# Optimization experiments

Measured on AMD Instinct MI355X. Metric: run time of the kernel, lower is better.

## Reference

```python
import jax, jax.numpy as jnp
import numpy as np

B, N, K = 16, 2048, 16        # events, nodes per event, neighbors
F_IN, L = 64, 64              # in_size, layer_size
EPS = 1e-5                    # BatchNorm1d eps


def setup_inputs() -> dict:
    key = jax.random.key(0)
    k1, k2 = jax.random.split(key, 2)
    x = jax.random.normal(k1, (B * N, F_IN), jnp.float32)
    batch = jnp.repeat(jnp.arange(B, dtype=jnp.int32), N)  # equal-size events
    W = jax.random.normal(k2, (2 * F_IN, L), jnp.float32) * 0.08
    b = jnp.zeros((L,), jnp.float32)
    gamma = jnp.ones((L,), jnp.float32)
    beta = jnp.zeros((L,), jnp.float32)
    return {"x": x, "batch": batch, "W": W, "b": b, "gamma": gamma, "beta": beta}


def reference(x, batch, W, b, gamma, beta):
    # batch encodes B equal-size events -> reshape to [B, N, F]
    xr = x.reshape(B, N, F_IN)

    # dynamic kNN in feature space, per event (self included, as in PyG knn)
    sq = jnp.sum(xr * xr, axis=-1)                                  # [B, N]
    d = sq[:, :, None] + sq[:, None, :] - 2.0 * jnp.einsum(
        'bnf,bmf->bnm', xr, xr)                                     # [B, N, N]
    _, idx = jax.lax.top_k(-d, K)                                   # [B, N, K]

    # gather neighbor features
    xj = jax.vmap(lambda xe, ie: xe[ie])(xr, idx)                   # [B, N, K, F]
    xi = jnp.broadcast_to(xr[:, :, None, :], (B, N, K, F_IN))

    # EdgeConv message: nn(cat([x_i, x_j - x_i]))
    e = jnp.concatenate([xi, xj - xi], axis=-1)                     # [B, N, K, 2F]
    h = jnp.einsum('bnke,el->bnkl', e, W) + b                       # Linear

    # BatchNorm1d over all edges (training-mode batch stats, biased var)
    m = jnp.mean(h, axis=(0, 1, 2))
    v = jnp.var(h, axis=(0, 1, 2))
    h = (h - m) * jax.lax.rsqrt(v + EPS) * gamma + beta
    h = jax.nn.relu(h)

    # aggr='mean' over the K neighbors
    out = jnp.mean(h, axis=2)                                       # [B, N, L]
    return out.reshape(B * N, L)
```

## Files before the change

### kernel.cpp

```cpp
#include <hip/hip_runtime.h>
#include <hip/hip_fp16.h>
#include <math.h>

#define B_EV    16
#define N_NODES 2048
#define K_NN    16
#define F_IN    64
#define L_OUT   64
#define NT      (B_EV * N_NODES)
#define EDGES   (NT * K_NN)

typedef __attribute__((ext_vector_type(8)))  short bh8;
typedef __attribute__((ext_vector_type(16))) float f32x16;
typedef __attribute__((ext_vector_type(8)))  unsigned short us8;

__device__ inline unsigned short bf16_rne(float f) {
  unsigned int u = __float_as_uint(f);
  return (unsigned short)((u + 0x7FFFu + ((u >> 16) & 1u)) >> 16);
}
__device__ inline float bf16f(unsigned short h) {
  return __uint_as_float(((unsigned int)h) << 16);
}

__device__ inline void gload16(const void* g, void* l) {
  __builtin_amdgcn_global_load_lds(
      (const __attribute__((address_space(1))) void*)(g),
      (__attribute__((address_space(3))) void*)(l), 16, 0, 0);
}

__global__ __launch_bounds__(256) void k_uv(const float* __restrict__ x,
                                            const float* __restrict__ W,
                                            float* __restrict__ u,
                                            float* __restrict__ v,
                                            float* __restrict__ sq,
                                            unsigned short* __restrict__ xh,
                                            unsigned short* __restrict__ xl) {
  __shared__ float xs[64][64];
  const int t = threadIdx.x;
  const int l = t & 63, g = t >> 6;
  const int nodeBase = blockIdx.x * 64;

  {
    const float4* gx = (const float4*)(x + (size_t)nodeBase * 64);
    float4* lx = (float4*)&xs[0][0];
    #pragma unroll
    for (int p = 0; p < 4; ++p) lx[p * 256 + t] = gx[p * 256 + t];
  }
  float wdc[64], w2c[64];
  #pragma unroll
  for (int f = 0; f < 64; ++f) {
    float w1v = W[f * 64 + l];
    float w2v = W[4096 + f * 64 + l];
    wdc[f] = w1v - w2v;
    w2c[f] = w2v;
  }
  __syncthreads();

  #pragma unroll
  for (int p = 0; p < 2; ++p) {
    int n = p * 32 + (t >> 3), j = t & 7;
    float xv = xs[n][j];
    float s = __fmul_rn(xv, xv);
    #pragma unroll
    for (int i = 1; i < 8; ++i) {
      float c = xs[n][j + 8 * i];
      s = __fadd_rn(s, __fmul_rn(c, c));
    }
    s = __fadd_rn(s, __shfl_xor(s, 1));
    s = __fadd_rn(s, __shfl_xor(s, 2));
    s = __fadd_rn(s, __shfl_xor(s, 4));
    if (j == 0) sq[nodeBase + n] = s;
  }
  #pragma unroll
  for (int p = 0; p < 4; ++p) {
    int i = p * 256 + t;
    float4 vv = ((const float4*)&xs[0][0])[i];
    ushort4 h, lo;
    h.x = bf16_rne(vv.x); lo.x = bf16_rne(vv.x - bf16f(h.x));
    h.y = bf16_rne(vv.y); lo.y = bf16_rne(vv.y - bf16f(h.y));
    h.z = bf16_rne(vv.z); lo.z = bf16_rne(vv.z - bf16f(h.z));
    h.w = bf16_rne(vv.w); lo.w = bf16_rne(vv.w - bf16f(h.w));
    ((ushort4*)xh)[(size_t)nodeBase * 16 + i] = h;
    ((ushort4*)xl)[(size_t)nodeBase * 16 + i] = lo;
  }

  for (int rep = 0; rep < 16; ++rep) {
    int n = rep * 4 + g;
    const float4* xr = (const float4*)xs[n];
    float au = 0.f, av = 0.f;
    #pragma unroll
    for (int fq = 0; fq < 16; ++fq) {
      float4 xv = xr[fq];
      au = fmaf(xv.x, wdc[fq * 4 + 0], au); av = fmaf(xv.x, w2c[fq * 4 + 0], av);
      au = fmaf(xv.y, wdc[fq * 4 + 1], au); av = fmaf(xv.y, w2c[fq * 4 + 1], av);
      au = fmaf(xv.z, wdc[fq * 4 + 2], au); av = fmaf(xv.z, w2c[fq * 4 + 2], av);
      au = fmaf(xv.w, wdc[fq * 4 + 3], au); av = fmaf(xv.w, w2c[fq * 4 + 3], av);
    }
    u[(size_t)(nodeBase + n) * 64 + l] = au;
    v[(size_t)(nodeBase + n) * 64 + l] = av;
  }
}

__global__ __launch_bounds__(256, 6) void k_gemm(const unsigned short* __restrict__ xh,
                                                 const unsigned short* __restrict__ xl,
                                                 const float* __restrict__ sq,
                                                 unsigned short* __restrict__ Sbuf,
                                                 int evBase) {
  __shared__ char xb[16384];
  __shared__ __align__(16) unsigned short Sh[32 * 128];
  const int t    = threadIdx.x;
  const int w    = t >> 6;
  const int lane = t & 63;
  const int ev    = evBase + (blockIdx.x >> 7);
  const int rem   = blockIdx.x & 127;
  const int strip = rem >> 1;
  const int half  = rem & 1;
  const int rowBase = strip * 32;
  const int T0 = half * 8;
  const size_t evNode = (size_t)ev * N_NODES;
  const float* __restrict__ sqev = sq + evNode;
  unsigned short* __restrict__ Sev =
      Sbuf + (size_t)(ev - evBase) * N_NODES * N_NODES;
  char* Sc = (char*)Sh;

  {
    int col = t >> 3;
    int fbs = ((t & 7) << 4) ^ ((col & 7) << 4);
    gload16((const char*)(xh + (evNode + rowBase + col) * 64) + fbs, Sc + t * 16);
    gload16((const char*)(xl + (evNode + rowBase + col) * 64) + fbs, Sc + 4096 + t * 16);
    #pragma unroll
    for (int p = 0; p < 4; ++p) {
      const int colB = p * 32 + (t >> 3);
      const char* g = (const char*)(xh + (evNode + T0 * 128 + colB) * 64) + fbs;
      gload16(g, xb + p * 4096 + t * 16);
    }
  }
  __syncthreads();
  bh8 ah[4], al[4];
  {
    int row = lane & 31;
    int fb  = (lane >> 5) * 16;
    #pragma unroll
    for (int ks = 0; ks < 4; ++ks) {
      int off = (row * 128 + ks * 32 + fb) ^ ((row & 7) << 4);
      ah[ks] = *(const bh8*)(Sc + off);
      al[ks] = *(const bh8*)(Sc + 4096 + off);
    }
  }
  __syncthreads();

  for (int T = T0; T < T0 + 8; ++T) {
    const int tileCol = T * 128;
    {
      f32x16 acc;
      #pragma unroll
      for (int q = 0; q < 16; ++q) acc[q] = 0.f;
      int colIn = w * 32 + (lane & 31);
      int fb = (lane >> 5) * 16;
      #pragma unroll
      for (int ks = 0; ks < 4; ++ks) {
        int off = (colIn * 128 + ks * 32 + fb) ^ ((colIn & 7) << 4);
        bh8 bh = *(const bh8*)(xb + off);
        acc = __builtin_amdgcn_mfma_f32_32x32x16_bf16(ah[ks], bh, acc, 0, 0, 0);
        acc = __builtin_amdgcn_mfma_f32_32x32x16_bf16(al[ks], bh, acc, 0, 0, 0);
      }
      float sqc = sqev[tileCol + colIn];
      #pragma unroll
      for (int reg = 0; reg < 16; ++reg) {
        int m = (reg & 3) + 8 * (reg >> 2) + 4 * (lane >> 5);
        Sh[m * 128 + colIn] =
            __half_as_ushort(__float2half(fmaf(-2.0f, acc[reg], sqc)));
      }
    }
    __syncthreads();
    if (T < T0 + 7) {
      #pragma unroll
      for (int p = 0; p < 4; ++p) {
        const int colB = p * 32 + (t >> 3);
        const int fbs = ((t & 7) << 4) ^ (((t >> 3) & 7) << 4);
        const char* g = (const char*)(xh + (evNode + tileCol + 128 + colB) * 64) + fbs;
        gload16(g, xb + p * 4096 + t * 16);
      }
    }
    {
      int r  = t >> 3;
      int cg = t & 7;
      unsigned short* gS =
          Sev + (size_t)(rowBase + r) * N_NODES + tileCol + cg * 16;
      const uint4* lS = (const uint4*)(Sh + r * 128 + cg * 16);
      *(uint4*)gS = lS[0];
      *(uint4*)(gS + 8) = lS[1];
    }
    __syncthreads();
  }
}

#define SCR_CAP 192
#define SEL_DELTA 1.0f

__global__ __launch_bounds__(256, 1) void k_sel(const float* __restrict__ x,
                                                const float* __restrict__ sq,
                                                const unsigned short* __restrict__ Sbuf,
                                                int* __restrict__ nidx,
                                                int rowBase) {
  __shared__ float xiS[4][64];
  __shared__ int candLDS[4][SCR_CAP];
  __shared__ unsigned long long keysLDS[4][SCR_CAP];
  const int w = threadIdx.x >> 6, lane = threadIdx.x & 63;
  const int rowInChunk = blockIdx.x * 4 + w;
  const int grow = rowBase + rowInChunk;
  const int ev = grow >> 11;
  const int rowInEv = grow & 2047;
  const size_t evNode = (size_t)ev * N_NODES;
  const unsigned short* __restrict__ Srow = Sbuf + (size_t)rowInChunk * N_NODES;
  const float* __restrict__ sqev = sq + evNode;
  const float* __restrict__ xev = x + evNode * F_IN;

  xiS[w][lane] = x[(evNode + rowInEv) * F_IN + lane];

  us8 pk[4];
  #pragma unroll
  for (int q = 0; q < 4; ++q)
    pk[q] = *(const us8*)(Srow + q * 512 + lane * 8);

  float mn = 3.4e38f;
  #pragma unroll
  for (int q = 0; q < 4; ++q) {
    #pragma unroll
    for (int e = 0; e < 8; ++e)
      mn = fminf(mn, __half2float(__ushort_as_half(pk[q][e])));
  }
  #pragma unroll
  for (int k = 2; k <= 64; k <<= 1) {
    #pragma unroll
    for (int j = k >> 1; j >= 1; j >>= 1) {
      float o = __shfl_xor(mn, j);
      bool up = ((lane & k) == 0);
      bool iAmLower = ((lane & j) == 0);
      bool wantSmall = (up == iAmLower);
      bool less = (mn < o);
      if (less != wantSmall) mn = o;
    }
  }
  const float thr = __shfl(mn, 15) + SEL_DELTA;

  unsigned int msk[4];
  int c = 0;
  #pragma unroll
  for (int q = 0; q < 4; ++q) {
    unsigned int m = 0;
    #pragma unroll
    for (int e = 0; e < 8; ++e) {
      float v = __half2float(__ushort_as_half(pk[q][e]));
      m |= (v <= thr) ? (1u << e) : 0u;
    }
    msk[q] = m;
    c += __popc(m);
  }
  int incl = c;
  #pragma unroll
  for (int off = 1; off < 64; off <<= 1) {
    int n = __shfl_up(incl, off);
    if (lane >= off) incl += n;
  }
  int pos = incl - c;
  int total = __shfl(incl, 63);
  const int cn = (total < SCR_CAP) ? total : SCR_CAP;
  #pragma unroll
  for (int q = 0; q < 4; ++q) {
    unsigned int m = msk[q];
    while (m) {
      int e = __ffs(m) - 1;
      m &= m - 1;
      if (pos < SCR_CAP) candLDS[w][pos] = q * 512 + lane * 8 + e;
      ++pos;
    }
  }

  const float sqn = sqev[rowInEv];
  const float* xiW = xiS[w];
  const int* crow = candLDS[w];

  int base = 0;
  while (base < cn) {
    int rem = cn - base;
    if (rem <= 32) {
      int hf = lane >> 5;
      int ii = lane & 31;
      int ci = base + ii;
      bool act = ii < rem;
      int mcol = act ? crow[ci] : 0;
      const float4* xm = (const float4*)(xev + (size_t)mcol * F_IN);
      double d0 = 0.0, d1 = 0.0;
      #pragma unroll
      for (int q = 0; q < 8; ++q) {
        int fq = hf * 8 + q;
        float4 cc = xm[fq];
        float4 xq = *(const float4*)(xiW + fq * 4);
        d0 = fma((double)xq.x, (double)cc.x, d0);
        d1 = fma((double)xq.y, (double)cc.y, d1);
        d0 = fma((double)xq.z, (double)cc.z, d0);
        d1 = fma((double)xq.w, (double)cc.w, d1);
      }
      double ds = d0 + d1;
      double od = __shfl_xor(ds, 32);
      if (act && hf == 0) {
        float dot32 = (float)(ds + od);
        float sv = __fsub_rn(__fadd_rn(sqn, sqev[mcol]), __fmul_rn(2.0f, dot32));
        unsigned int fb = __float_as_uint(sv);
        fb = (fb & 0x80000000u) ? ~fb : (fb | 0x80000000u);
        keysLDS[w][ci] = ((unsigned long long)fb << 32) | (unsigned int)mcol;
      }
      base = cn;
    } else {
      int ci = base + lane;
      bool act = ci < cn;
      int mcol = act ? crow[ci] : 0;
      const float4* xm = (const float4*)(xev + (size_t)mcol * F_IN);
      double d0 = 0.0, d1 = 0.0, d2 = 0.0, d3 = 0.0;
      #pragma unroll
      for (int fq = 0; fq < 16; fq += 4) {
        float4 c0 = xm[fq + 0], c1 = xm[fq + 1], c2 = xm[fq + 2], c3 = xm[fq + 3];
        float4 x0 = *(const float4*)(xiW + fq * 4);
        float4 x1 = *(const float4*)(xiW + fq * 4 + 4);
        float4 x2 = *(const float4*)(xiW + fq * 4 + 8);
        float4 x3 = *(const float4*)(xiW + fq * 4 + 12);
        d0 = fma((double)x0.x, (double)c0.x, d0);
        d0 = fma((double)x0.y, (double)c0.y, d0);
        d0 = fma((double)x0.z, (double)c0.z, d0);
        d0 = fma((double)x0.w, (double)c0.w, d0);
        d1 = fma((double)x1.x, (double)c1.x, d1);
        d1 = fma((double)x1.y, (double)c1.y, d1);
        d1 = fma((double)x1.z, (double)c1.z, d1);
        d1 = fma((double)x1.w, (double)c1.w, d1);
        d2 = fma((double)x2.x, (double)c2.x, d2);
        d2 = fma((double)x2.y, (double)c2.y, d2);
        d2 = fma((double)x2.z, (double)c2.z, d2);
        d2 = fma((double)x2.w, (double)c2.w, d2);
        d3 = fma((double)x3.x, (double)c3.x, d3);
        d3 = fma((double)x3.y, (double)c3.y, d3);
        d3 = fma((double)x3.z, (double)c3.z, d3);
        d3 = fma((double)x3.w, (double)c3.w, d3);
      }
      if (act) {
        float dot32 = (float)((d0 + d1) + (d2 + d3));
        float sv = __fsub_rn(__fadd_rn(sqn, sqev[mcol]), __fmul_rn(2.0f, dot32));
        unsigned int fb = __float_as_uint(sv);
        fb = (fb & 0x80000000u) ? ~fb : (fb | 0x80000000u);
        keysLDS[w][ci] = ((unsigned long long)fb << 32) | (unsigned int)mcol;
      }
      base += 64;
    }
  }

  const unsigned long long INVALID = ~0ull;
  unsigned long long k0 = INVALID, k1 = INVALID, k2 = INVALID;
  if (lane < cn)        k0 = keysLDS[w][lane];
  if (lane + 64 < cn)   k1 = keysLDS[w][lane + 64];
  if (lane + 128 < cn)  k2 = keysLDS[w][lane + 128];
  int r0 = 0, r1 = 0, r2 = 0;
  for (int i = 0; i < cn; ++i) {
    unsigned long long kk = keysLDS[w][i];
    r0 += (kk < k0) ? 1 : 0;
    r1 += (kk < k1) ? 1 : 0;
    r2 += (kk < k2) ? 1 : 0;
  }
  const size_t outBase = (evNode + rowInEv) * K_NN;
  if (lane < cn && r0 < K_NN)
    nidx[outBase + r0] = (int)evNode + (int)(k0 & 0x7FFFFFFFu);
  if (lane + 64 < cn && r1 < K_NN)
    nidx[outBase + r1] = (int)evNode + (int)(k1 & 0x7FFFFFFFu);
  if (lane + 128 < cn && r2 < K_NN)
    nidx[outBase + r2] = (int)evNode + (int)(k2 & 0x7FFFFFFFu);
}

#define NS 16
#define NC 128
union KnnSmem {
  struct {
    char  xb[32768];
    float S[32 * 129];
  } a;
  struct {
    float sc[32][NC + 1];
    int   id[32][NC + 1];
    int   cand[32][24];
    float resc[32][24];
  } b;
};

__global__ __launch_bounds__(256, 3) void k_knn(const float* __restrict__ x,
                                                const unsigned short* __restrict__ xh,
                                                const unsigned short* __restrict__ xl,
                                                const float* __restrict__ sq,
                                                int* __restrict__ nidx) {
  __shared__ KnnSmem sm;
  const int t    = threadIdx.x;
  const int r    = t & 31;
  const int c8   = t >> 5;
  const int w    = t >> 6;
  const int lane = t & 63;
  const int ev    = blockIdx.x >> 6;
  const int strip = blockIdx.x & 63;
  const int rowBase = strip * 32;
  const size_t evNode = (size_t)ev * N_NODES;
  const float* __restrict__ sqev = sq + evNode;

  {
    int col = t >> 3;
    int fb  = (t & 7) << 4;
    const char* gh = (const char*)(xh + (evNode + rowBase + col) * 64) + fb;
    const char* gl = (const char*)(xl + (evNode + rowBase + col) * 64) + fb;
    int off = (col * 128 + fb) ^ ((col & 7) << 4);
    *(uint4*)(sm.a.xb + off)         = *(const uint4*)gh;
    *(uint4*)(sm.a.xb + 16384 + off) = *(const uint4*)gl;
  }
  __syncthreads();
  bh8 ah[4], al[4];
  {
    int row = lane & 31;
    int fb  = (lane >> 5) * 16;
    #pragma unroll
    for (int ks = 0; ks < 4; ++ks) {
      int off = (row * 128 + ks * 32 + fb) ^ ((row & 7) << 4);
      ah[ks] = *(const bh8*)(sm.a.xb + off);
      al[ks] = *(const bh8*)(sm.a.xb + 16384 + off);
    }
  }

  float dist[NS]; int idxk[NS];
  #pragma unroll
  for (int q = 0; q < NS; ++q) { dist[q] = 3.4e38f; idxk[q] = 0x7FFFFFFF; }
  float curMax = 3.4e38f;

  for (int T = 0; T < 16; ++T) {
    __syncthreads();
    const int tileCol = T * 128;
    #pragma unroll
    for (int p = 0; p < 8; ++p) {
      int idx16 = (p & 3) * 256 + t;
      int col = idx16 >> 3;
      int fb  = (idx16 & 7) << 4;
      const unsigned short* src = (p < 4) ? xh : xl;
      const char* g = (const char*)(src + (evNode + tileCol + col) * 64) + fb;
      int off = ((p < 4) ? 0 : 16384) + ((col * 128 + fb) ^ ((col & 7) << 4));
      *(uint4*)(sm.a.xb + off) = *(const uint4*)g;
    }
    __syncthreads();
    {
      f32x16 acc;
      #pragma unroll
      for (int q = 0; q < 16; ++q) acc[q] = 0.f;
      int colIn = w * 32 + (lane & 31);
      int fb = (lane >> 5) * 16;
      #pragma unroll
      for (int ks = 0; ks < 4; ++ks) {
        int off = (colIn * 128 + ks * 32 + fb) ^ ((colIn & 7) << 4);
        bh8 bh = *(const bh8*)(sm.a.xb + off);
        bh8 bl = *(const bh8*)(sm.a.xb + 16384 + off);
        acc = __builtin_amdgcn_mfma_f32_32x32x16_bf16(ah[ks], bh, acc, 0, 0, 0);
        acc = __builtin_amdgcn_mfma_f32_32x32x16_bf16(ah[ks], bl, acc, 0, 0, 0);
        acc = __builtin_amdgcn_mfma_f32_32x32x16_bf16(al[ks], bh, acc, 0, 0, 0);
      }
      float sqc = sqev[tileCol + colIn];
      #pragma unroll
      for (int reg = 0; reg < 16; ++reg) {
        int m = (reg & 3) + 8 * (reg >> 2) + 4 * (lane >> 5);
        sm.a.S[m * 129 + colIn] = fmaf(-2.0f, acc[reg], sqc);
      }
    }
    __syncthreads();
    for (int j = 0; j < 16; ++j) {
      int cIn = c8 * 16 + j;
      float s = sm.a.S[r * 129 + cIn];
      if (s <= curMax) {
        int col = tileCol + cIn;
        float bv = dist[0]; int bi = idxk[0]; int slot = 0;
        #pragma unroll
        for (int q = 1; q < NS; ++q) {
          bool worse = (dist[q] > bv) || ((dist[q] == bv) && (idxk[q] > bi));
          slot = worse ? q : slot;
          bv = worse ? dist[q] : bv;
          bi = worse ? idxk[q] : bi;
        }
        if ((s < bv) || ((s == bv) && (col < bi))) {
          #pragma unroll
          for (int q = 0; q < NS; ++q) {
            dist[q] = (q == slot) ? s : dist[q];
            idxk[q] = (q == slot) ? col : idxk[q];
          }
          float cm = dist[0];
          #pragma unroll
          for (int q = 1; q < NS; ++q) cm = fmaxf(cm, dist[q]);
          curMax = cm;
        }
      }
    }
  }

  __syncthreads();
  #pragma unroll
  for (int q = 0; q < NS; ++q) {
    sm.b.sc[r][c8 * NS + q] = dist[q];
    sm.b.id[r][c8 * NS + q] = idxk[q];
  }
  __syncthreads();

  if (t < 32) {
    float dd[24]; int di[24];
    #pragma unroll
    for (int q = 0; q < 24; ++q) { dd[q] = 3.4e38f; di[q] = 0x7FFFFFFF; }
    for (int c = 0; c < NC; ++c) {
      float s = sm.b.sc[t][c];
      int m = sm.b.id[t][c];
      float bv = dd[0]; int bi = di[0]; int slot = 0;
      #pragma unroll
      for (int q = 1; q < 24; ++q) {
        bool worse = (dd[q] > bv) || ((dd[q] == bv) && (di[q] > bi));
        slot = worse ? q : slot;
        bv = worse ? dd[q] : bv;
        bi = worse ? di[q] : bi;
      }
      if ((s < bv) || ((s == bv) && (m < bi))) {
        #pragma unroll
        for (int q = 0; q < 24; ++q) {
          dd[q] = (q == slot) ? s : dd[q];
          di[q] = (q == slot) ? m : di[q];
        }
      }
    }
    #pragma unroll
    for (int q = 0; q < 24; ++q) sm.b.cand[t][q] = di[q];
  }
  __syncthreads();

  {
    float4 xi[16];
    const float4* xr = (const float4*)(x + (evNode + rowBase + r) * F_IN);
    #pragma unroll
    for (int fq = 0; fq < 16; ++fq) xi[fq] = xr[fq];
    const float sqn = sqev[rowBase + r];
    const float* __restrict__ xev = x + evNode * F_IN;
    #pragma unroll
    for (int ii = 0; ii < 3; ++ii) {
      int i = c8 + ii * 8;
      int m = sm.b.cand[r][i];
      const float4* xm = (const float4*)(xev + (size_t)m * F_IN);
      double dot = 0.0;
      #pragma unroll
      for (int fq = 0; fq < 16; ++fq) {
        float4 cc = xm[fq];
        dot = fma((double)xi[fq].x, (double)cc.x, dot);
        dot = fma((double)xi[fq].y, (double)cc.y, dot);
        dot = fma((double)xi[fq].z, (double)cc.z, dot);
        dot = fma((double)xi[fq].w, (double)cc.w, dot);
      }
      const float dot32 = (float)dot;
      sm.b.resc[r][i] = __fsub_rn(__fadd_rn(sqn, sqev[m]),
                                  __fmul_rn(2.0f, dot32));
    }
  }
  __syncthreads();

  if (t < 32) {
    float dd[K_NN]; int di[K_NN];
    #pragma unroll
    for (int q = 0; q < K_NN; ++q) { dd[q] = 3.4e38f; di[q] = 0x7FFFFFFF; }
    for (int c = 0; c < 24; ++c) {
      float s = sm.b.resc[t][c];
      int m = sm.b.cand[t][c];
      float bv = dd[0]; int bi = di[0]; int slot = 0;
      #pragma unroll
      for (int q = 1; q < K_NN; ++q) {
        bool worse = (dd[q] > bv) || ((dd[q] == bv) && (di[q] > bi));
        slot = worse ? q : slot;
        bv = worse ? dd[q] : bv;
        bi = worse ? di[q] : bi;
      }
      if ((s < bv) || ((s == bv) && (m < bi))) {
        #pragma unroll
        for (int q = 0; q < K_NN; ++q) {
          dd[q] = (q == slot) ? s : dd[q];
          di[q] = (q == slot) ? m : di[q];
        }
      }
    }
    const size_t row = evNode + rowBase + t;
    #pragma unroll
    for (int q = 0; q < K_NN; ++q)
      nidx[row * K_NN + q] = (int)evNode + di[q];
  }
}

#define NB_ST 32
__global__ __launch_bounds__(256) void k_stats(const float* __restrict__ u,
                                               const float* __restrict__ v,
                                               const int* __restrict__ nidx,
                                               const float* __restrict__ bvec,
                                               float* __restrict__ stats) {
  __shared__ float red1[4][64];
  __shared__ float red2[4][64];
  const int l = threadIdx.x & 63, g = threadIdx.x >> 6;
  const int base = blockIdx.x * NB_ST;
  const float bl = bvec[l];
  float s1 = 0.f, s2 = 0.f;
  for (int nn = g; nn < NB_ST; nn += 4) {
    const int node = base + nn;
    const float ui = u[(size_t)node * 64 + l] + bl;
    const int* ip = nidx + (size_t)node * K_NN;
    int idx[16];
    #pragma unroll
    for (int q = 0; q < 4; ++q)
      *(int4*)&idx[q * 4] = *(const int4*)(ip + q * 4);
    #pragma unroll
    for (int k = 0; k < K_NN; ++k) {
      const float vj = v[(size_t)idx[k] * 64 + l];
      const float h = ui + vj;
      s1 += h;
      s2 = fmaf(h, h, s2);
    }
  }
  red1[g][l] = s1; red2[g][l] = s2;
  __syncthreads();
  if (g == 0) {
    float t1 = red1[0][l] + red1[1][l] + red1[2][l] + red1[3][l];
    float t2 = red2[0][l] + red2[1][l] + red2[2][l] + red2[3][l];
    atomicAdd(&stats[l], t1);
    atomicAdd(&stats[64 + l], t2);
  }
}

__global__ __launch_bounds__(256) void k_out(const float* __restrict__ u,
                                             const float* __restrict__ v,
                                             const int* __restrict__ nidx,
                                             const float* __restrict__ bvec,
                                             const float* __restrict__ gamma,
                                             const float* __restrict__ beta,
                                             const float* __restrict__ stats,
                                             float* __restrict__ out) {
  const int l = threadIdx.x & 63, g = threadIdx.x >> 6;
  const float inv = 1.0f / (float)EDGES;
  const float mean = stats[l] * inv;
  const float ex2 = stats[64 + l] * inv;
  const float var = ex2 - mean * mean;
  const float a = gamma[l] * rsqrtf(var + 1e-5f);
  const float bb = fmaf(-mean, a, beta[l]);
  const float bl = bvec[l];
  const int base = blockIdx.x * NB_ST;
  for (int nn = g; nn < NB_ST; nn += 4) {
    const int node = base + nn;
    const float ui = u[(size_t)node * 64 + l] + bl;
    const int* ip = nidx + (size_t)node * K_NN;
    int idx[16];
    #pragma unroll
    for (int q = 0; q < 4; ++q)
      *(int4*)&idx[q * 4] = *(const int4*)(ip + q * 4);
    float acc = 0.f;
    #pragma unroll
    for (int k = 0; k < K_NN; ++k) {
      const float vj = v[(size_t)idx[k] * 64 + l];
      const float h = ui + vj;
      acc += fmaxf(fmaf(a, h, bb), 0.f);
    }
    out[(size_t)node * 64 + l] = acc * (1.0f / 16.0f);
  }
}

extern "C" void kernel_launch(void* const* d_in, const int* in_sizes, int n_in,
                              void* d_out, int out_size, void* d_ws, size_t ws_size,
                              hipStream_t stream) {
  (void)in_sizes; (void)n_in; (void)out_size;
  const float* x     = (const float*)d_in[0];
  const float* W     = (const float*)d_in[2];
  const float* b     = (const float*)d_in[3];
  const float* gamma = (const float*)d_in[4];
  const float* beta  = (const float*)d_in[5];
  float* out = (float*)d_out;

  char* ws = (char*)d_ws;
  float*          u     = (float*)(ws);
  float*          v     = (float*)(ws + 8388608);
  float*          sq    = (float*)(ws + 16777216);
  int*            nidx  = (int*)  (ws + 16908288);
  float*          stats = (float*)(ws + 19005440);
  unsigned short* xh    = (unsigned short*)(ws + 19005952);
  unsigned short* xl    = (unsigned short*)(ws + 23200256);
  unsigned short* Sbuf  = (unsigned short*)(ws + 27394560);

  const size_t sChunkBytes = (size_t)N_NODES * N_NODES * 2;
  size_t avail = (ws_size > 27394560) ? ws_size - 27394560 : 0;
  int evCap = (int)((avail / sChunkBytes < 16) ? (avail / sChunkBytes) : 16);

  hipMemsetAsync(stats, 0, 512, stream);
  k_uv  <<<512, 256, 0, stream>>>(x, W, u, v, sq, xh, xl);

  if (evCap >= 1) {
    for (int e0 = 0; e0 < B_EV; e0 += evCap) {
      int ne = (B_EV - e0 < evCap) ? (B_EV - e0) : evCap;
      k_gemm<<<ne * 128, 256, 0, stream>>>(xh, xl, sq, Sbuf, e0);
      k_sel <<<ne * 512, 256, 0, stream>>>(x, sq, Sbuf, nidx, e0 * N_NODES);
    }
  } else {
    k_knn<<<1024, 256, 0, stream>>>(x, xh, xl, sq, nidx);
  }

  k_stats<<<1024, 256, 0, stream>>>(u, v, nidx, b, stats);
  k_out <<<1024, 256, 0, stream>>>(u, v, nidx, b, gamma, beta, stats, out);
}
```

Before: 174.0 us.

## Process two rows per wavefront in k_sel to fill lanes during rescoring

Each wavefront in the selection kernel now handles two adjacent rows instead of one. When both rows have at most 32 candidates, the two half-waves rescore them at the same time in fp64, rather than splitting one row's dot products across halves. The grid is halved, the interleaved min, threshold and scan steps add instruction-level parallelism, and the scoring code moves into a shared helper. In exchange, register and LDS use per wave rise and the number of waves in flight drops.

```diff
diff --git a/kernel.cpp b/kernel.cpp
--- a/kernel.cpp
+++ b/kernel.cpp
@@ -26,6 +26,43 @@
   __builtin_amdgcn_global_load_lds(
       (const __attribute__((address_space(1))) void*)(g),
       (__attribute__((address_space(3))) void*)(l), 16, 0, 0);
+}
+
+__device__ inline unsigned long long score_key(const float* xiW,
+                                               const float* __restrict__ xev,
+                                               int mcol, float sqn,
+                                               const float* __restrict__ sqev) {
+  const float4* xm = (const float4*)(xev + (size_t)mcol * F_IN);
+  double d0 = 0.0, d1 = 0.0, d2 = 0.0, d3 = 0.0;
+  #pragma unroll
+  for (int fq = 0; fq < 16; fq += 4) {
+    float4 c0 = xm[fq + 0], c1 = xm[fq + 1], c2 = xm[fq + 2], c3 = xm[fq + 3];
+    float4 x0 = *(const float4*)(xiW + fq * 4);
+    float4 x1 = *(const float4*)(xiW + fq * 4 + 4);
+    float4 x2 = *(const float4*)(xiW + fq * 4 + 8);
+    float4 x3 = *(const float4*)(xiW + fq * 4 + 12);
+    d0 = fma((double)x0.x, (double)c0.x, d0);
+    d0 = fma((double)x0.y, (double)c0.y, d0);
+    d0 = fma((double)x0.z, (double)c0.z, d0);
+    d0 = fma((double)x0.w, (double)c0.w, d0);
+    d1 = fma((double)x1.x, (double)c1.x, d1);
+    d1 = fma((double)x1.y, (double)c1.y, d1);
+    d1 = fma((double)x1.z, (double)c1.z, d1);
+    d1 = fma((double)x1.w, (double)c1.w, d1);
+    d2 = fma((double)x2.x, (double)c2.x, d2);
+    d2 = fma((double)x2.y, (double)c2.y, d2);
+    d2 = fma((double)x2.z, (double)c2.z, d2);
+    d2 = fma((double)x2.w, (double)c2.w, d2);
+    d3 = fma((double)x3.x, (double)c3.x, d3);
+    d3 = fma((double)x3.y, (double)c3.y, d3);
+    d3 = fma((double)x3.z, (double)c3.z, d3);
+    d3 = fma((double)x3.w, (double)c3.w, d3);
+  }
+  float dot32 = (float)((d0 + d1) + (d2 + d3));
+  float sv = __fsub_rn(__fadd_rn(sqn, sqev[mcol]), __fmul_rn(2.0f, dot32));
+  unsigned int fb = __float_as_uint(sv);
+  fb = (fb & 0x80000000u) ? ~fb : (fb | 0x80000000u);
+  return ((unsigned long long)fb << 32) | (unsigned int)mcol;
 }
 
 __global__ __launch_bounds__(256) void k_uv(const float* __restrict__ x,
@@ -203,175 +240,165 @@
                                                 const unsigned short* __restrict__ Sbuf,
                                                 int* __restrict__ nidx,
                                                 int rowBase) {
-  __shared__ float xiS[4][64];
-  __shared__ int candLDS[4][SCR_CAP];
-  __shared__ unsigned long long keysLDS[4][SCR_CAP];
+  __shared__ float xiS[4][2][64];
+  __shared__ int candLDS[4][2][SCR_CAP];
+  __shared__ unsigned long long keysLDS[4][2][SCR_CAP];
   const int w = threadIdx.x >> 6, lane = threadIdx.x & 63;
-  const int rowInChunk = blockIdx.x * 4 + w;
-  const int grow = rowBase + rowInChunk;
-  const int ev = grow >> 11;
-  const int rowInEv = grow & 2047;
+  const int pair = blockIdx.x * 4 + w;
+  const int ricA = pair * 2;
+  const int growA = rowBase + ricA;
+  const int ev = growA >> 11;
+  const int rieA = growA & 2047;
   const size_t evNode = (size_t)ev * N_NODES;
-  const unsigned short* __restrict__ Srow = Sbuf + (size_t)rowInChunk * N_NODES;
+  const unsigned short* __restrict__ SrowA = Sbuf + (size_t)ricA * N_NODES;
+  const unsigned short* __restrict__ SrowB = SrowA + N_NODES;
   const float* __restrict__ sqev = sq + evNode;
   const float* __restrict__ xev = x + evNode * F_IN;
 
-  xiS[w][lane] = x[(evNode + rowInEv) * F_IN + lane];
-
-  us8 pk[4];
-  #pragma unroll
-  for (int q = 0; q < 4; ++q)
-    pk[q] = *(const us8*)(Srow + q * 512 + lane * 8);
-
-  float mn = 3.4e38f;
+  xiS[w][0][lane] = x[(evNode + rieA) * F_IN + lane];
+  xiS[w][1][lane] = x[(evNode + rieA + 1) * F_IN + lane];
+
+  us8 pa[4], pb[4];
   #pragma unroll
   for (int q = 0; q < 4; ++q) {
-    #pragma unroll
-    for (int e = 0; e < 8; ++e)
-      mn = fminf(mn, __half2float(__ushort_as_half(pk[q][e])));
+    pa[q] = *(const us8*)(SrowA + q * 512 + lane * 8);
+    pb[q] = *(const us8*)(SrowB + q * 512 + lane * 8);
+  }
+  float mna = 3.4e38f, mnb = 3.4e38f;
+  #pragma unroll
+  for (int q = 0; q < 4; ++q) {
+    #pragma unroll
+    for (int e = 0; e < 8; ++e) {
+      mna = fminf(mna, __half2float(__ushort_as_half(pa[q][e])));
+      mnb = fminf(mnb, __half2float(__ushort_as_half(pb[q][e])));
+    }
   }
   #pragma unroll
   for (int k = 2; k <= 64; k <<= 1) {
     #pragma unroll
     for (int j = k >> 1; j >= 1; j >>= 1) {
-      float o = __shfl_xor(mn, j);
+      float oa = __shfl_xor(mna, j);
+      float ob = __shfl_xor(mnb, j);
       bool up = ((lane & k) == 0);
       bool iAmLower = ((lane & j) == 0);
       bool wantSmall = (up == iAmLower);
-      bool less = (mn < o);
-      if (less != wantSmall) mn = o;
-    }
-  }
-  const float thr = __shfl(mn, 15) + SEL_DELTA;
-
-  unsigned int msk[4];
-  int c = 0;
+      if ((mna < oa) != wantSmall) mna = oa;
+      if ((mnb < ob) != wantSmall) mnb = ob;
+    }
+  }
+  const float thrA = __shfl(mna, 15) + SEL_DELTA;
+  const float thrB = __shfl(mnb, 15) + SEL_DELTA;
+
+  unsigned int mskA[4], mskB[4];
+  int ca = 0, cb = 0;
   #pragma unroll
   for (int q = 0; q < 4; ++q) {
-    unsigned int m = 0;
+    unsigned int ma = 0, mb = 0;
     #pragma unroll
     for (int e = 0; e < 8; ++e) {
-      float v = __half2float(__ushort_as_half(pk[q][e]));
-      m |= (v <= thr) ? (1u << e) : 0u;
-    }
-    msk[q] = m;
-    c += __popc(m);
-  }
-  int incl = c;
+      ma |= (__half2float(__ushort_as_half(pa[q][e])) <= thrA) ? (1u << e) : 0u;
+      mb |= (__half2float(__ushort_as_half(pb[q][e])) <= thrB) ? (1u << e) : 0u;
+    }
+    mskA[q] = ma; mskB[q] = mb;
+    ca += __popc(ma); cb += __popc(mb);
+  }
+  int incla = ca, inclb = cb;
   #pragma unroll
   for (int off = 1; off < 64; off <<= 1) {
-    int n = __shfl_up(incl, off);
-    if (lane >= off) incl += n;
-  }
-  int pos = incl - c;
-  int total = __shfl(incl, 63);
-  const int cn = (total < SCR_CAP) ? total : SCR_CAP;
+    int na = __shfl_up(incla, off);
+    int nb = __shfl_up(inclb, off);
+    if (lane >= off) { incla += na; inclb += nb; }
+  }
+  int posA = incla - ca, posB = inclb - cb;
+  int totalA = __shfl(incla, 63), totalB = __shfl(inclb, 63);
+  const int cnA = (totalA < SCR_CAP) ? totalA : SCR_CAP;
+  const int cnB = (totalB < SCR_CAP) ? totalB : SCR_CAP;
   #pragma unroll
   for (int q = 0; q < 4; ++q) {
-    unsigned int m = msk[q];
+    unsigned int m = mskA[q];
     while (m) {
-      int e = __ffs(m) - 1;
-      m &= m - 1;
-      if (pos < SCR_CAP) candLDS[w][pos] = q * 512 + lane * 8 + e;
-      ++pos;
-    }
-  }
-
-  const float sqn = sqev[rowInEv];
-  const float* xiW = xiS[w];
-  const int* crow = candLDS[w];
-
-  int base = 0;
-  while (base < cn) {
-    int rem = cn - base;
-    if (rem <= 32) {
-      int hf = lane >> 5;
-      int ii = lane & 31;
-      int ci = base + ii;
-      bool act = ii < rem;
-      int mcol = act ? crow[ci] : 0;
-      const float4* xm = (const float4*)(xev + (size_t)mcol * F_IN);
-      double d0 = 0.0, d1 = 0.0;
-      #pragma unroll
-      for (int q = 0; q < 8; ++q) {
-        int fq = hf * 8 + q;
-        float4 cc = xm[fq];
-        float4 xq = *(const float4*)(xiW + fq * 4);
-        d0 = fma((double)xq.x, (double)cc.x, d0);
-        d1 = fma((double)xq.y, (double)cc.y, d1);
-        d0 = fma((double)xq.z, (double)cc.z, d0);
-        d1 = fma((double)xq.w, (double)cc.w, d1);
-      }
-      double ds = d0 + d1;
-      double od = __shfl_xor(ds, 32);
-      if (act && hf == 0) {
-        float dot32 = (float)(ds + od);
-        float sv = __fsub_rn(__fadd_rn(sqn, sqev[mcol]), __fmul_rn(2.0f, dot32));
-        unsigned int fb = __float_as_uint(sv);
-        fb = (fb & 0x80000000u) ? ~fb : (fb | 0x80000000u);
-        keysLDS[w][ci] = ((unsigned long long)fb << 32) | (unsigned int)mcol;
-      }
-      base = cn;
-    } else {
-      int ci = base + lane;
-      bool act = ci < cn;
-      int mcol = act ? crow[ci] : 0;
-      const float4* xm = (const float4*)(xev + (size_t)mcol * F_IN);
-      double d0 = 0.0, d1 = 0.0, d2 = 0.0, d3 = 0.0;
-      #pragma unroll
-      for (int fq = 0; fq < 16; fq += 4) {
-        float4 c0 = xm[fq + 0], c1 = xm[fq + 1], c2 = xm[fq + 2], c3 = xm[fq + 3];
-        float4 x0 = *(const float4*)(xiW + fq * 4);
-        float4 x1 = *(const float4*)(xiW + fq * 4 + 4);
-        float4 x2 = *(const float4*)(xiW + fq * 4 + 8);
-        float4 x3 = *(const float4*)(xiW + fq * 4 + 12);
-        d0 = fma((double)x0.x, (double)c0.x, d0);
-        d0 = fma((double)x0.y, (double)c0.y, d0);
-        d0 = fma((double)x0.z, (double)c0.z, d0);
-        d0 = fma((double)x0.w, (double)c0.w, d0);
-        d1 = fma((double)x1.x, (double)c1.x, d1);
-        d1 = fma((double)x1.y, (double)c1.y, d1);
-        d1 = fma((double)x1.z, (double)c1.z, d1);
-        d1 = fma((double)x1.w, (double)c1.w, d1);
-        d2 = fma((double)x2.x, (double)c2.x, d2);
-        d2 = fma((double)x2.y, (double)c2.y, d2);
-        d2 = fma((double)x2.z, (double)c2.z, d2);
-        d2 = fma((double)x2.w, (double)c2.w, d2);
-        d3 = fma((double)x3.x, (double)c3.x, d3);
-        d3 = fma((double)x3.y, (double)c3.y, d3);
-        d3 = fma((double)x3.z, (double)c3.z, d3);
-        d3 = fma((double)x3.w, (double)c3.w, d3);
-      }
-      if (act) {
-        float dot32 = (float)((d0 + d1) + (d2 + d3));
-        float sv = __fsub_rn(__fadd_rn(sqn, sqev[mcol]), __fmul_rn(2.0f, dot32));
-        unsigned int fb = __float_as_uint(sv);
-        fb = (fb & 0x80000000u) ? ~fb : (fb | 0x80000000u);
-        keysLDS[w][ci] = ((unsigned long long)fb << 32) | (unsigned int)mcol;
-      }
-      base += 64;
+      int e = __ffs(m) - 1; m &= m - 1;
+      if (posA < SCR_CAP) candLDS[w][0][posA] = q * 512 + lane * 8 + e;
+      ++posA;
+    }
+    m = mskB[q];
+    while (m) {
+      int e = __ffs(m) - 1; m &= m - 1;
+      if (posB < SCR_CAP) candLDS[w][1][posB] = q * 512 + lane * 8 + e;
+      ++posB;
+    }
+  }
+
+  const float sqnA = sqev[rieA];
+  const float sqnB = sqev[rieA + 1];
+
+  if (cnA <= 32 && cnB <= 32) {
+    const int which = lane >> 5;
+    const int ii = lane & 31;
+    const int cnW = which ? cnB : cnA;
+    const bool act = ii < cnW;
+    const int mcol = act ? candLDS[w][which][ii] : 0;
+    const float* xiW = xiS[w][which];
+    const float sqnW = which ? sqnB : sqnA;
+    unsigned long long key = score_key(xiW, xev, mcol, sqnW, sqev);
+    if (act) keysLDS[w][which][ii] = key;
+  } else {
+    #pragma unroll 1
+    for (int rr = 0; rr < 2; ++rr) {
+      const int cnW = rr ? cnB : cnA;
+      const float* xiW = xiS[w][rr];
+      const float sqnW = rr ? sqnB : sqnA;
+      for (int bs = 0; bs < cnW; bs += 64) {
+        int ci = bs + lane;
+        bool act = ci < cnW;
+        int mcol = act ? candLDS[w][rr][ci] : 0;
+        unsigned long long key = score_key(xiW, xev, mcol, sqnW, sqev);
+        if (act) keysLDS[w][rr][ci] = key;
+      }
     }
   }
 
   const unsigned long long INVALID = ~0ull;
-  unsigned long long k0 = INVALID, k1 = INVALID, k2 = INVALID;
-  if (lane < cn)        k0 = keysLDS[w][lane];
-  if (lane + 64 < cn)   k1 = keysLDS[w][lane + 64];
-  if (lane + 128 < cn)  k2 = keysLDS[w][lane + 128];
-  int r0 = 0, r1 = 0, r2 = 0;
-  for (int i = 0; i < cn; ++i) {
-    unsigned long long kk = keysLDS[w][i];
-    r0 += (kk < k0) ? 1 : 0;
-    r1 += (kk < k1) ? 1 : 0;
-    r2 += (kk < k2) ? 1 : 0;
-  }
-  const size_t outBase = (evNode + rowInEv) * K_NN;
-  if (lane < cn && r0 < K_NN)
-    nidx[outBase + r0] = (int)evNode + (int)(k0 & 0x7FFFFFFFu);
-  if (lane + 64 < cn && r1 < K_NN)
-    nidx[outBase + r1] = (int)evNode + (int)(k1 & 0x7FFFFFFFu);
-  if (lane + 128 < cn && r2 < K_NN)
-    nidx[outBase + r2] = (int)evNode + (int)(k2 & 0x7FFFFFFFu);
+  {
+    unsigned long long k0 = INVALID, k1 = INVALID, k2 = INVALID;
+    if (lane < cnA)       k0 = keysLDS[w][0][lane];
+    if (lane + 64 < cnA)  k1 = keysLDS[w][0][lane + 64];
+    if (lane + 128 < cnA) k2 = keysLDS[w][0][lane + 128];
+    int r0 = 0, r1 = 0, r2 = 0;
+    for (int i = 0; i < cnA; ++i) {
+      unsigned long long kk = keysLDS[w][0][i];
+      r0 += (kk < k0) ? 1 : 0;
+      r1 += (kk < k1) ? 1 : 0;
+      r2 += (kk < k2) ? 1 : 0;
+    }
+    const size_t outBase = (evNode + rieA) * K_NN;
+    if (lane < cnA && r0 < K_NN)
+      nidx[outBase + r0] = (int)evNode + (int)(k0 & 0x7FFFFFFFu);
+    if (lane + 64 < cnA && r1 < K_NN)
+      nidx[outBase + r1] = (int)evNode + (int)(k1 & 0x7FFFFFFFu);
+    if (lane + 128 < cnA && r2 < K_NN)
+      nidx[outBase + r2] = (int)evNode + (int)(k2 & 0x7FFFFFFFu);
+  }
+  {
+    unsigned long long k0 = INVALID, k1 = INVALID, k2 = INVALID;
+    if (lane < cnB)       k0 = keysLDS[w][1][lane];
+    if (lane + 64 < cnB)  k1 = keysLDS[w][1][lane + 64];
+    if (lane + 128 < cnB) k2 = keysLDS[w][1][lane + 128];
+    int r0 = 0, r1 = 0, r2 = 0;
+    for (int i = 0; i < cnB; ++i) {
+      unsigned long long kk = keysLDS[w][1][i];
+      r0 += (kk < k0) ? 1 : 0;
+      r1 += (kk < k1) ? 1 : 0;
+      r2 += (kk < k2) ? 1 : 0;
+    }
+    const size_t outBase = (evNode + rieA + 1) * K_NN;
+    if (lane < cnB && r0 < K_NN)
+      nidx[outBase + r0] = (int)evNode + (int)(k0 & 0x7FFFFFFFu);
+    if (lane + 64 < cnB && r1 < K_NN)
+      nidx[outBase + r1] = (int)evNode + (int)(k1 & 0x7FFFFFFFu);
+    if (lane + 128 < cnB && r2 < K_NN)
+      nidx[outBase + r2] = (int)evNode + (int)(k2 & 0x7FFFFFFFu);
+  }
 }
 
 #define NS 16
@@ -698,7 +725,7 @@
     for (int e0 = 0; e0 < B_EV; e0 += evCap) {
       int ne = (B_EV - e0 < evCap) ? (B_EV - e0) : evCap;
       k_gemm<<<ne * 128, 256, 0, stream>>>(xh, xl, sq, Sbuf, e0);
-      k_sel <<<ne * 512, 256, 0, stream>>>(x, sq, Sbuf, nidx, e0 * N_NODES);
+      k_sel <<<ne * 256, 256, 0, stream>>>(x, sq, Sbuf, nidx, e0 * N_NODES);
     }
   } else {
     k_knn<<<1024, 256, 0, stream>>>(x, xh, xl, sq, nidx);
```

New measurement: 175.4 us. No clear change (+0.8%).
